# Kernel tuning notes

Measured on AMD Instinct MI355X. Metric: run time of the kernel, lower is better.

Reference implementation:

```python
import jax, jax.numpy as jnp
import numpy as np

B, T, F, H, OUT = 256, 256, 128, 1024, 128


def setup_inputs() -> dict:
    key = jax.random.key(0)
    ks = jax.random.split(key, 6)
    s_ih = 1.0 / np.sqrt(H)
    return {
        "x": jax.random.normal(ks[0], (B, T, F), dtype=jnp.float32),
        "h0": jnp.zeros((B, H), dtype=jnp.float32),
        "c0": jnp.zeros((B, H), dtype=jnp.float32),
        "W_ih": jax.random.normal(ks[1], (4 * H, F), dtype=jnp.float32) * s_ih,
        "W_hh": jax.random.normal(ks[2], (4 * H, H), dtype=jnp.float32) * s_ih,
        "b_ih": jax.random.normal(ks[3], (4 * H,), dtype=jnp.float32) * s_ih,
        "b_hh": jax.random.normal(ks[4], (4 * H,), dtype=jnp.float32) * s_ih,
        "W_fc": jax.random.normal(ks[5], (OUT, H), dtype=jnp.float32) * s_ih,
        "b_fc": jnp.zeros((OUT,), dtype=jnp.float32),
    }


def _lstm_scan(x, h0, c0, W_ih, W_hh, b_ih, b_hh):
    # Precompute input projections for all timesteps: [T, B, 4H]
    x_t = jnp.swapaxes(x, 0, 1)  # [T, B, F]
    x_proj = jnp.einsum('tbf,gf->tbg', x_t, W_ih) + b_ih + b_hh

    def step(carry, xp):
        h, c = carry
        gates = xp + h @ W_hh.T  # [B, 4H]
        i, f, g, o = jnp.split(gates, 4, axis=-1)  # PyTorch LSTMCell gate order
        i = jax.nn.sigmoid(i)
        f = jax.nn.sigmoid(f)
        g = jnp.tanh(g)
        o = jax.nn.sigmoid(o)
        c = f * c + i * g
        h = o * jnp.tanh(c)
        return (h, c), None

    (h, c), _ = jax.lax.scan(step, (h0, c0), x_proj)
    return h, c


def reference(x, h0, c0, W_ih, W_hh, b_ih, b_hh, W_fc, b_fc):
    h, c = _lstm_scan(x, h0, c0, W_ih, W_hh, b_ih, b_hh)
    sig_out = jax.nn.sigmoid(h)
    # Dropout is identity in eval/reference mode
    return sig_out @ W_fc.T + b_fc  # [B, OUT]
```

## Files before the change

kernel.cpp:

```cpp
#include <hip/hip_runtime.h>


typedef _Float16 f16x8 __attribute__((ext_vector_type(8)));
typedef float f32x16 __attribute__((ext_vector_type(16)));
typedef unsigned long long u64;

#define SCOPE_AGENT __HIP_MEMORY_SCOPE_AGENT

#define WS_WP    0ull
#define WS_BIAS  9437184ull
#define WS_XT    (WS_BIAS + 16384ull)
#define WS_HB    (WS_XT + 16777216ull)
#define WS_SIGH  (WS_HB + 4ull * 262144ull)
#define WS_BAR   (WS_SIGH + 1048576ull)

__device__ __forceinline__ unsigned short f2h(float f) {
  _Float16 h = (_Float16)f;
  return __builtin_bit_cast(unsigned short, h);
}

__device__ __forceinline__ float fast_sig(float x) {
  return __builtin_amdgcn_rcpf(1.f + __expf(-x));
}
__device__ __forceinline__ float fast_tanh(float x) {
  return __builtin_fmaf(2.f, fast_sig(2.f * x), -1.f);
}

__device__ __forceinline__ unsigned char h_enc(float v) {
  _Float16 gh = (_Float16)(v * 0.00390625f);
  unsigned m = __builtin_bit_cast(unsigned short, gh);
  unsigned r = m + 0x3fu + ((m >> 7) & 1u);
  return (unsigned char)(((m >> 8) & 0x80u) | ((r >> 7) & 0x7fu));
}

__device__ __forceinline__ f16x8 dq(u64 v) {
  unsigned w0 = (unsigned)v, w1 = (unsigned)(v >> 32);
  unsigned e0 = w0 & 0x00ff00ffu, o0 = (w0 >> 8) & 0x00ff00ffu;
  unsigned e1 = w1 & 0x00ff00ffu, o1 = (w1 >> 8) & 0x00ff00ffu;
  int4 t;
  t.x = (int)((e0 + (e0 & 0x00800080u)) << 7);
  t.y = (int)((o0 + (o0 & 0x00800080u)) << 7);
  t.z = (int)((e1 + (e1 & 0x00800080u)) << 7);
  t.w = (int)((o1 + (o1 & 0x00800080u)) << 7);
  return __builtin_bit_cast(f16x8, t);
}

__global__ void prep_pack(const float* __restrict__ W_ih, const float* __restrict__ W_hh,
                          const float* __restrict__ b_ih, const float* __restrict__ b_hh,
                          unsigned short* __restrict__ wp, float* __restrict__ bias) {
  unsigned i = blockIdx.x * 256u + threadIdx.x;
  if (i < 4718592u) {
    unsigned j = i & 7u;
    unsigned l = (i >> 3) & 63u;
    unsigned rest = i >> 9;
    unsigned q = rest % 18u;
    unsigned rest2 = rest / 18u;
    unsigned n = rest2 & 3u;
    unsigned rest3 = rest2 >> 2;
    unsigned w = rest3 & 3u;
    unsigned cg = rest3 >> 2;
    unsigned gcol = n * 1024u + cg * 32u + (l & 31u);
    unsigned khi = (l >> 5) * 8u;
    float v;
    if (q < 16u) {
      unsigned pj = (0x75643120u >> (4u * j)) & 0xfu;
      unsigned k = w * 256u + q * 16u + khi + pj;
      v = W_hh[(size_t)gcol * 1024u + k];
    } else {
      unsigned k = w * 32u + (q - 16u) * 16u + khi + j;
      v = W_ih[(size_t)gcol * 128u + k];
    }
    wp[i] = f2h(v * 256.0f);
  }
  if (i < 4096u) bias[i] = b_ih[i] + b_hh[i];
}

__global__ void prep_misc(const float* __restrict__ x, const float* __restrict__ h0,
                          unsigned short* __restrict__ xT, unsigned char* __restrict__ hb0,
                          unsigned* __restrict__ bar) {
  unsigned i = blockIdx.x * 256u + threadIdx.x;
  if (i < 8388608u) {
    unsigned f = i & 127u;
    unsigned b = (i >> 7) & 255u;
    unsigned t = i >> 15;
    xT[i] = f2h(x[((size_t)b * 256u + t) * 128u + f] * 0.00390625f);
  }
  if (i < 262144u) hb0[i] = h_enc(h0[i]);
  if (i < 768u) bar[i] = 0u;
}

__launch_bounds__(256, 1)
__global__ void lstm_main(const unsigned short* __restrict__ wp,
                          const float* __restrict__ bias,
                          const unsigned short* __restrict__ xT,
                          unsigned char* __restrict__ hb,
                          const float* __restrict__ c0,
                          float* __restrict__ sigh,
                          unsigned* __restrict__ bar) {
  extern __shared__ char lds[];
  char* stg = lds;
  float4* redv = (float4*)(lds + 32768);
  unsigned char* hst8 = (unsigned char*)(lds + 98304);

  const unsigned tid = threadIdx.x;
  const unsigned wg  = blockIdx.x;
  const unsigned w   = tid >> 6;
  const unsigned l   = tid & 63u;
  const unsigned rg  = wg >> 5;
  const unsigned cg  = wg & 31u;
  const unsigned lo5 = l & 31u;
  const unsigned hi  = l >> 5;

  int4 Braw[4][18];
  {
    const int4* wpv = (const int4*)wp;
    const unsigned wbase = (cg * 4u + w) * 4608u;
#pragma unroll
    for (int n = 0; n < 4; ++n) {
#pragma unroll
      for (int q = 0; q < 18; ++q) {
        Braw[n][q] = wpv[wbase + (unsigned)(n * 18 + q) * 64u + l];
      }
    }
  }

  float bias_v[4];
#pragma unroll
  for (int n = 0; n < 4; ++n) bias_v[n] = bias[(unsigned)n * 1024u + cg * 32u + lo5];

  const unsigned col = cg * 32u + lo5;
  float c_st[4];
  unsigned soff[4];
#pragma unroll
  for (int i = 0; i < 4; ++i) {
    unsigned r = rg * 32u + 8u * w + (unsigned)i + 4u * hi;
    soff[i] = r * 1024u + col;
    c_st[i] = c0[soff[i]];
  }

  const unsigned sgsrc0 = (rg * 32u + hi) * 1024u + w * 256u + lo5 * 8u;
  const unsigned sdst0  = w * 8192u + hi * 256u + lo5 * 8u;
  const unsigned frb = w * 8192u + lo5 * 256u + hi * 8u;
  const unsigned fxr = (lo5 & 7u) << 3;

  unsigned xb = ((rg * 32u + lo5) * 128u + w * 32u + hi * 8u) * 2u;

  const char* xbase = (const char*)xT;
  char* hbase = (char*)hb;
  unsigned* flags = &bar[rg * 32u];

  const unsigned srow = tid >> 3;
  const unsigned sseg = tid & 7u;
  const unsigned sgoff = (rg * 32u + srow) * 1024u + cg * 32u + sseg * 4u;

  int4 xr[2];
  xr[0] = *(const int4*)(xbase + xb);
  xr[1] = *(const int4*)(xbase + xb + 32u);

  for (unsigned t = 0; t < 256u; ++t) {
    const char* hrd = hbase + ((t & 3u) * 262144u);
    char* hwr = hbase + (((t + 1u) & 3u) * 262144u);

    u64 sa[16];
#pragma unroll
    for (int r = 0; r < 16; ++r)
      sa[r] = __hip_atomic_load((const u64*)(hrd + sgsrc0 + (unsigned)r * 2048u),
                                __ATOMIC_RELAXED, SCOPE_AGENT);

    f32x16 acc[4] = {};
#pragma unroll
    for (int qx = 0; qx < 2; ++qx) {
      f16x8 a = __builtin_bit_cast(f16x8, xr[qx]);
      acc[0] = __builtin_amdgcn_mfma_f32_32x32x16_f16(a, __builtin_bit_cast(f16x8, Braw[0][16 + qx]), acc[0], 0, 0, 0);
      acc[1] = __builtin_amdgcn_mfma_f32_32x32x16_f16(a, __builtin_bit_cast(f16x8, Braw[1][16 + qx]), acc[1], 0, 0, 0);
      acc[2] = __builtin_amdgcn_mfma_f32_32x32x16_f16(a, __builtin_bit_cast(f16x8, Braw[2][16 + qx]), acc[2], 0, 0, 0);
      acc[3] = __builtin_amdgcn_mfma_f32_32x32x16_f16(a, __builtin_bit_cast(f16x8, Braw[3][16 + qx]), acc[3], 0, 0, 0);
    }

#pragma unroll
    for (int r = 0; r < 16; ++r) {
      unsigned d = sdst0 + (unsigned)r * 512u;
      unsigned a = d ^ (((d >> 8) & 7u) << 3);
      *(u64*)(stg + a) = sa[r];
    }
    asm volatile("s_waitcnt lgkmcnt(0)" ::: "memory");

#pragma unroll
    for (int q = 0; q < 16; ++q) {
      unsigned a2 = (frb + (unsigned)q * 16u) ^ fxr;
      u64 hv = *(const u64*)(stg + a2);
      f16x8 a = dq(hv);
      acc[0] = __builtin_amdgcn_mfma_f32_32x32x16_f16(a, __builtin_bit_cast(f16x8, Braw[0][q]), acc[0], 0, 0, 0);
      acc[1] = __builtin_amdgcn_mfma_f32_32x32x16_f16(a, __builtin_bit_cast(f16x8, Braw[1][q]), acc[1], 0, 0, 0);
      acc[2] = __builtin_amdgcn_mfma_f32_32x32x16_f16(a, __builtin_bit_cast(f16x8, Braw[2][q]), acc[2], 0, 0, 0);
      acc[3] = __builtin_amdgcn_mfma_f32_32x32x16_f16(a, __builtin_bit_cast(f16x8, Braw[3][q]), acc[3], 0, 0, 0);
    }

#pragma unroll
    for (int n = 0; n < 4; ++n) {
#pragma unroll
      for (int c = 0; c < 4; ++c) {
        float4 v;
        v.x = acc[n][4 * c + 0]; v.y = acc[n][4 * c + 1];
        v.z = acc[n][4 * c + 2]; v.w = acc[n][4 * c + 3];
        redv[((w * 4u + (unsigned)n) * 4u + (unsigned)c) * 64u + l] = v;
      }
    }
    __syncthreads();

    float gv[4][4];
#pragma unroll
    for (int n = 0; n < 4; ++n) {
      float4 s; s.x = bias_v[n]; s.y = bias_v[n]; s.z = bias_v[n]; s.w = bias_v[n];
#pragma unroll
      for (int wo = 0; wo < 4; ++wo) {
        float4 v = redv[(((unsigned)wo * 4u + (unsigned)n) * 4u + w) * 64u + l];
        s.x += v.x; s.y += v.y; s.z += v.z; s.w += v.w;
      }
      gv[n][0] = s.x; gv[n][1] = s.y; gv[n][2] = s.z; gv[n][3] = s.w;
    }

    const bool last = (t == 255u);
#pragma unroll
    for (int i = 0; i < 4; ++i) {
      float ig = fast_sig(gv[0][i]);
      float fg = fast_sig(gv[1][i]);
      float gg = fast_tanh(gv[2][i]);
      float og = fast_sig(gv[3][i]);
      float cc = fg * c_st[i] + ig * gg;
      c_st[i] = cc;
      float hh = og * fast_tanh(cc);
      hst8[(8u * w + (unsigned)i + 4u * hi) * 32u + lo5] = h_enc(hh);
      if (last) sigh[soff[i]] = fast_sig(hh);
    }

    if (!last) {
      __syncthreads();
      {
        unsigned v = *(const unsigned*)(hst8 + srow * 32u + sseg * 4u);
        __hip_atomic_store((unsigned*)(hwr + sgoff), v, __ATOMIC_RELAXED, SCOPE_AGENT);
      }
      xb += 65536u;
      xr[0] = *(const int4*)(xbase + xb);
      xr[1] = *(const int4*)(xbase + xb + 32u);
      __syncthreads();
      if (tid == 0)
        __hip_atomic_store(&flags[cg], t + 1u, __ATOMIC_RELAXED, SCOPE_AGENT);
      {
        const unsigned tgt = t + 1u;
        const unsigned fidx = w * 8u + (l & 7u);
        for (;;) {
          unsigned f = __hip_atomic_load(&flags[fidx], __ATOMIC_RELAXED, SCOPE_AGENT);
          if (__all(f >= tgt)) break;
          __builtin_amdgcn_s_sleep(1);
        }
      }
    }
  }
}

__global__ void final_fc(const float* __restrict__ sigh, const float* __restrict__ W_fc,
                         const float* __restrict__ b_fc, float* __restrict__ out) {
  unsigned b = blockIdx.x;
  unsigned o = threadIdx.x;
  const float* hrow = sigh + (size_t)b * 1024u;
  const float* wrow = W_fc + (size_t)o * 1024u;
  float acc = b_fc[o];
#pragma unroll 8
  for (unsigned k = 0; k < 1024u; k += 4u) {
    float4 hv = *(const float4*)(hrow + k);
    float4 wv = *(const float4*)(wrow + k);
    acc += hv.x * wv.x + hv.y * wv.y + hv.z * wv.z + hv.w * wv.w;
  }
  out[b * 128u + o] = acc;
}

extern "C" void kernel_launch(void* const* d_in, const int* in_sizes, int n_in,
                              void* d_out, int out_size, void* d_ws, size_t ws_size,
                              hipStream_t stream) {
  (void)in_sizes; (void)n_in; (void)out_size; (void)ws_size;
  const float* x    = (const float*)d_in[0];
  const float* h0   = (const float*)d_in[1];
  const float* c0   = (const float*)d_in[2];
  const float* W_ih = (const float*)d_in[3];
  const float* W_hh = (const float*)d_in[4];
  const float* b_ih = (const float*)d_in[5];
  const float* b_hh = (const float*)d_in[6];
  const float* W_fc = (const float*)d_in[7];
  const float* b_fc = (const float*)d_in[8];

  char* ws = (char*)d_ws;
  unsigned short* wp   = (unsigned short*)(ws + WS_WP);
  float*          bias = (float*)(ws + WS_BIAS);
  unsigned short* xT   = (unsigned short*)(ws + WS_XT);
  unsigned char*  hb   = (unsigned char*)(ws + WS_HB);
  float*          sigh = (float*)(ws + WS_SIGH);
  unsigned*       bar  = (unsigned*)(ws + WS_BAR);
  float*          out  = (float*)d_out;

  prep_pack<<<18432, 256, 0, stream>>>(W_ih, W_hh, b_ih, b_hh, wp, bias);
  prep_misc<<<32768, 256, 0, stream>>>(x, h0, xT, hb, bar);
  lstm_main<<<256, 256, 99328, stream>>>(wp, bias, xT, hb, c0, sigh, bar);
  final_fc<<<256, 128, 0, stream>>>(sigh, W_fc, b_fc, out);
}
```

Baseline: 1.308 ms.

## Split batch into two interleaved halves with hash-verified speculative h reads

Each workgroup now processes two 16-row batch halves (A and B) in alternation, so the cross-workgroup exchange of one half overlaps with the compute of the other. The MFMA tiling changes from 32x32x16 to 16x16x32, and the weight packing is rearranged to match. The per-step flag barrier is replaced by speculative loads of the hidden-state tile, checked against a per-tile hash carrying the epoch. The code falls back to flag polling only when the hash does not match. The aim is to remove the global barrier latency from the recurrence's critical path. The cost is extra hashing arithmetic, and hash-based validation carries a small risk of a false match.

```diff
diff --git a/kernel.cpp b/kernel.cpp
--- a/kernel.cpp
+++ b/kernel.cpp
@@ -2,8 +2,9 @@
 
 
 typedef _Float16 f16x8 __attribute__((ext_vector_type(8)));
-typedef float f32x16 __attribute__((ext_vector_type(16)));
+typedef float f32x4 __attribute__((ext_vector_type(4)));
 typedef unsigned long long u64;
+typedef unsigned u32;
 
 #define SCOPE_AGENT __HIP_MEMORY_SCOPE_AGENT
 
@@ -11,28 +12,26 @@
 #define WS_BIAS  9437184ull
 #define WS_XT    (WS_BIAS + 16384ull)
 #define WS_HB    (WS_XT + 16777216ull)
-#define WS_SIGH  (WS_HB + 4ull * 262144ull)
+#define WS_HASH  (WS_HB + 1048576ull)
+#define WS_SIGH  (WS_HASH + 8192ull)
 #define WS_BAR   (WS_SIGH + 1048576ull)
 
 __device__ __forceinline__ unsigned short f2h(float f) {
   _Float16 h = (_Float16)f;
   return __builtin_bit_cast(unsigned short, h);
 }
-
 __device__ __forceinline__ float fast_sig(float x) {
   return __builtin_amdgcn_rcpf(1.f + __expf(-x));
 }
 __device__ __forceinline__ float fast_tanh(float x) {
   return __builtin_fmaf(2.f, fast_sig(2.f * x), -1.f);
 }
-
 __device__ __forceinline__ unsigned char h_enc(float v) {
   _Float16 gh = (_Float16)(v * 0.00390625f);
   unsigned m = __builtin_bit_cast(unsigned short, gh);
   unsigned r = m + 0x3fu + ((m >> 7) & 1u);
   return (unsigned char)(((m >> 8) & 0x80u) | ((r >> 7) & 0x7fu));
 }
-
 __device__ __forceinline__ f16x8 dq(u64 v) {
   unsigned w0 = (unsigned)v, w1 = (unsigned)(v >> 32);
   unsigned e0 = w0 & 0x00ff00ffu, o0 = (w0 >> 8) & 0x00ff00ffu;
@@ -45,6 +44,12 @@
   return __builtin_bit_cast(f16x8, t);
 }
 
+__device__ __forceinline__ u32 fold64(u64 v) {
+  return (u32)v ^ ((u32)(v >> 32) * 0x85EBCA77u);
+}
+#define HASH_INIT(EP, POS) (0x9E3779B9u * (u32)(EP) + (u32)(POS) * 0x7FEB352Du + 0x165667B1u)
+#define HASH_STEP(H, V, R)  ((((H) ^ fold64(V)) * 0x9E3779B1u) + (u32)(R))
+
 __global__ void prep_pack(const float* __restrict__ W_ih, const float* __restrict__ W_hh,
                           const float* __restrict__ b_ih, const float* __restrict__ b_hh,
                           unsigned short* __restrict__ wp, float* __restrict__ bias) {
@@ -53,22 +58,22 @@
     unsigned j = i & 7u;
     unsigned l = (i >> 3) & 63u;
     unsigned rest = i >> 9;
-    unsigned q = rest % 18u;
-    unsigned rest2 = rest / 18u;
-    unsigned n = rest2 & 3u;
-    unsigned rest3 = rest2 >> 2;
+    unsigned q = rest % 9u;
+    unsigned rest2 = rest / 9u;
+    unsigned ct = rest2 & 7u;
+    unsigned rest3 = rest2 >> 3;
     unsigned w = rest3 & 3u;
     unsigned cg = rest3 >> 2;
-    unsigned gcol = n * 1024u + cg * 32u + (l & 31u);
-    unsigned khi = (l >> 5) * 8u;
+    unsigned gcol = (ct >> 1) * 1024u + cg * 32u + (ct & 1u) * 16u + (l & 15u);
+    unsigned khi = (l >> 4) * 8u;
     float v;
-    if (q < 16u) {
+    if (q < 8u) {
       unsigned pj = (0x75643120u >> (4u * j)) & 0xfu;
-      unsigned k = w * 256u + q * 16u + khi + pj;
+      unsigned k = w * 256u + q * 32u + khi + pj;
       v = W_hh[(size_t)gcol * 1024u + k];
     } else {
-      unsigned k = w * 32u + (q - 16u) * 16u + khi + j;
-      v = W_ih[(size_t)gcol * 128u + k];
+      unsigned f = w * 32u + khi + j;
+      v = W_ih[(size_t)gcol * 128u + f];
     }
     wp[i] = f2h(v * 256.0f);
   }
@@ -76,7 +81,7 @@
 }
 
 __global__ void prep_misc(const float* __restrict__ x, const float* __restrict__ h0,
-                          unsigned short* __restrict__ xT, unsigned char* __restrict__ hb0,
+                          unsigned short* __restrict__ xT, unsigned char* __restrict__ hb,
                           unsigned* __restrict__ bar) {
   unsigned i = blockIdx.x * 256u + threadIdx.x;
   if (i < 8388608u) {
@@ -85,22 +90,76 @@
     unsigned t = i >> 15;
     xT[i] = f2h(x[((size_t)b * 256u + t) * 128u + f] * 0.00390625f);
   }
-  if (i < 262144u) hb0[i] = h_enc(h0[i]);
-  if (i < 768u) bar[i] = 0u;
-}
+  if (i < 262144u) {
+    unsigned col = i & 1023u;
+    unsigned grow = i >> 10;
+    unsigned g = grow >> 7;
+    unsigned rg = (grow >> 4) & 7u;
+    unsigned row = grow & 15u;
+    hb[((g * 4u + 0u) * 8u + rg) * 16384u + row * 1024u + col] = h_enc(h0[i]);
+  }
+  if (i < 512u) bar[i] = 0u;
+}
+
+__global__ void prep_hash(const unsigned char* __restrict__ hb, unsigned* __restrict__ hashes) {
+  unsigned id = blockIdx.x * 256u + threadIdx.x;
+  if (id >= 512u) return;
+  unsigned g = id >> 8, rg = (id >> 5) & 7u, cg = id & 31u;
+  const unsigned char* base = hb + ((g * 4u + 0u) * 8u + rg) * 16384u;
+  u32 tile = 0u;
+  for (unsigned pos = 0; pos < 8u; ++pos) {
+    u32 h = HASH_INIT(0u, pos);
+    for (unsigned r = 0; r < 8u; ++r) {
+      u64 v = *(const u64*)(base + ((pos >> 2) + 2u * r) * 1024u + cg * 32u + (pos & 3u) * 8u);
+      h = HASH_STEP(h, v, r);
+    }
+    tile ^= h;
+  }
+  hashes[((g * 4u + 0u) * 8u + rg) * 32u + cg] = tile;
+}
+
+#define SPEC_LOAD(SA, HA, G, SLOT) do {                                          \
+    const char* _b = (const char*)hbase + (((G)*4u + (SLOT))*8u + rg)*16384u     \
+                     + hi*1024u + w*256u + lo5*8u;                               \
+    for (int _r = 0; _r < 8; ++_r)                                               \
+      SA[_r] = __hip_atomic_load((const u64*)(_b + (unsigned)_r*2048u),          \
+                                 __ATOMIC_RELAXED, SCOPE_AGENT);                 \
+    HA = __hip_atomic_load(hashes + (((G)*4u + (SLOT))*8u + rg)*32u              \
+                           + w*8u + (lo5 >> 2), __ATOMIC_RELAXED, SCOPE_AGENT);  \
+  } while (0)
+
+#define VERIFY(SA, HA, EPOCH, OK) do {                                           \
+    u32 _h = HASH_INIT((EPOCH), pos);                                            \
+    for (int _r = 0; _r < 8; ++_r) _h = HASH_STEP(_h, SA[_r], _r);               \
+    _h ^= (u32)__shfl_xor((int)_h, 1, 64);                                       \
+    _h ^= (u32)__shfl_xor((int)_h, 2, 64);                                       \
+    _h ^= (u32)__shfl_xor((int)_h, 32, 64);                                      \
+    OK = __all(_h == (HA));                                                      \
+  } while (0)
+
+#define POLL(FL, TGT) do {                                                       \
+    for (;;) {                                                                   \
+      unsigned _f = __hip_atomic_load((FL) + w*8u + (l & 7u),                    \
+                                      __ATOMIC_RELAXED, SCOPE_AGENT);            \
+      if (__all(_f >= (TGT))) break;                                             \
+      __builtin_amdgcn_s_sleep(1);                                               \
+    }                                                                            \
+  } while (0)
 
 __launch_bounds__(256, 1)
 __global__ void lstm_main(const unsigned short* __restrict__ wp,
                           const float* __restrict__ bias,
                           const unsigned short* __restrict__ xT,
                           unsigned char* __restrict__ hb,
+                          unsigned* __restrict__ hashes,
                           const float* __restrict__ c0,
                           float* __restrict__ sigh,
                           unsigned* __restrict__ bar) {
   extern __shared__ char lds[];
-  char* stg = lds;
-  float4* redv = (float4*)(lds + 32768);
-  unsigned char* hst8 = (unsigned char*)(lds + 98304);
+  float4* redv = (float4*)(lds + 16384);
+  float*  redf = (float*)(lds + 16384);
+  unsigned char* hstA = (unsigned char*)(lds + 49152);
+  unsigned char* hstB = (unsigned char*)(lds + 49664);
 
   const unsigned tid = threadIdx.x;
   const unsigned wg  = blockIdx.x;
@@ -110,150 +169,228 @@
   const unsigned cg  = wg & 31u;
   const unsigned lo5 = l & 31u;
   const unsigned hi  = l >> 5;
-
-  int4 Braw[4][18];
+  const unsigned l15 = l & 15u;
+  const unsigned l4  = l >> 4;
+  const unsigned pos = (hi << 2) | (lo5 & 3u);
+  const unsigned row = l4 * 4u + w;
+
+  int4 Braw[8][9];
   {
     const int4* wpv = (const int4*)wp;
     const unsigned wbase = (cg * 4u + w) * 4608u;
 #pragma unroll
-    for (int n = 0; n < 4; ++n) {
-#pragma unroll
-      for (int q = 0; q < 18; ++q) {
-        Braw[n][q] = wpv[wbase + (unsigned)(n * 18 + q) * 64u + l];
-      }
-    }
-  }
-
-  float bias_v[4];
-#pragma unroll
-  for (int n = 0; n < 4; ++n) bias_v[n] = bias[(unsigned)n * 1024u + cg * 32u + lo5];
-
-  const unsigned col = cg * 32u + lo5;
-  float c_st[4];
-  unsigned soff[4];
-#pragma unroll
-  for (int i = 0; i < 4; ++i) {
-    unsigned r = rg * 32u + 8u * w + (unsigned)i + 4u * hi;
-    soff[i] = r * 1024u + col;
-    c_st[i] = c0[soff[i]];
-  }
-
-  const unsigned sgsrc0 = (rg * 32u + hi) * 1024u + w * 256u + lo5 * 8u;
-  const unsigned sdst0  = w * 8192u + hi * 256u + lo5 * 8u;
-  const unsigned frb = w * 8192u + lo5 * 256u + hi * 8u;
-  const unsigned fxr = (lo5 & 7u) << 3;
-
-  unsigned xb = ((rg * 32u + lo5) * 128u + w * 32u + hi * 8u) * 2u;
+    for (int ct = 0; ct < 8; ++ct)
+#pragma unroll
+      for (int q = 0; q < 9; ++q)
+        Braw[ct][q] = wpv[wbase + (unsigned)(ct * 9 + q) * 64u + l];
+  }
+
+  float bias_v[8];
+#pragma unroll
+  for (int ct = 0; ct < 8; ++ct)
+    bias_v[ct] = bias[(unsigned)(ct >> 1) * 1024u + cg * 32u + (unsigned)(ct & 1) * 16u + l15];
+
+  const unsigned gbA = rg * 16u, gbB = 128u + rg * 16u;
+  float cA[2], cB[2];
+  unsigned soffA[2], soffB[2];
+#pragma unroll
+  for (int hh = 0; hh < 2; ++hh) {
+    soffA[hh] = (gbA + row) * 1024u + cg * 32u + (unsigned)hh * 16u + l15;
+    soffB[hh] = (gbB + row) * 1024u + cg * 32u + (unsigned)hh * 16u + l15;
+    cA[hh] = c0[soffA[hh]];
+    cB[hh] = c0[soffB[hh]];
+  }
 
   const char* xbase = (const char*)xT;
-  char* hbase = (char*)hb;
-  unsigned* flags = &bar[rg * 32u];
-
-  const unsigned srow = tid >> 3;
-  const unsigned sseg = tid & 7u;
-  const unsigned sgoff = (rg * 32u + srow) * 1024u + cg * 32u + sseg * 4u;
-
-  int4 xr[2];
-  xr[0] = *(const int4*)(xbase + xb);
-  xr[1] = *(const int4*)(xbase + xb + 32u);
+  const unsigned xoffA = ((gbA + l15) * 128u + w * 32u + l4 * 8u) * 2u;
+  const unsigned xoffB = ((gbB + l15) * 128u + w * 32u + l4 * 8u) * 2u;
+  unsigned char* hbase = hb;
+  unsigned* flagsA = &bar[rg * 32u];
+  unsigned* flagsB = &bar[256u + rg * 32u];
+
+  const unsigned fb = w * 4096u + l15 * 256u + l4 * 8u;
+  const unsigned fx = (l15 & 7u) << 3;
+
+  u64 saA[8], saB[8];
+  u32 haA, haB;
+  int4 xrA, xrB;
+
+  SPEC_LOAD(saA, haA, 0u, 0u);
+  xrA = *(const int4*)(xbase + xoffA);
+  xrB = *(const int4*)(xbase + xoffB);
 
   for (unsigned t = 0; t < 256u; ++t) {
-    const char* hrd = hbase + ((t & 3u) * 262144u);
-    char* hwr = hbase + (((t + 1u) & 3u) * 262144u);
-
-    u64 sa[16];
-#pragma unroll
-    for (int r = 0; r < 16; ++r)
-      sa[r] = __hip_atomic_load((const u64*)(hrd + sgsrc0 + (unsigned)r * 2048u),
-                                __ATOMIC_RELAXED, SCOPE_AGENT);
-
-    f32x16 acc[4] = {};
-#pragma unroll
-    for (int qx = 0; qx < 2; ++qx) {
-      f16x8 a = __builtin_bit_cast(f16x8, xr[qx]);
-      acc[0] = __builtin_amdgcn_mfma_f32_32x32x16_f16(a, __builtin_bit_cast(f16x8, Braw[0][16 + qx]), acc[0], 0, 0, 0);
-      acc[1] = __builtin_amdgcn_mfma_f32_32x32x16_f16(a, __builtin_bit_cast(f16x8, Braw[1][16 + qx]), acc[1], 0, 0, 0);
-      acc[2] = __builtin_amdgcn_mfma_f32_32x32x16_f16(a, __builtin_bit_cast(f16x8, Braw[2][16 + qx]), acc[2], 0, 0, 0);
-      acc[3] = __builtin_amdgcn_mfma_f32_32x32x16_f16(a, __builtin_bit_cast(f16x8, Braw[3][16 + qx]), acc[3], 0, 0, 0);
-    }
-
-#pragma unroll
-    for (int r = 0; r < 16; ++r) {
-      unsigned d = sdst0 + (unsigned)r * 512u;
-      unsigned a = d ^ (((d >> 8) & 7u) << 3);
-      *(u64*)(stg + a) = sa[r];
-    }
-    asm volatile("s_waitcnt lgkmcnt(0)" ::: "memory");
-
-#pragma unroll
-    for (int q = 0; q < 16; ++q) {
-      unsigned a2 = (frb + (unsigned)q * 16u) ^ fxr;
-      u64 hv = *(const u64*)(stg + a2);
+    const bool last = (t == 255u);
+    const unsigned slot = t & 3u, wslot = (t + 1u) & 3u;
+
+    {
+      bool ok; VERIFY(saA, haA, t, ok);
+      if (!ok) {
+        SPEC_LOAD(saA, haA, 0u, slot);
+        VERIFY(saA, haA, t, ok);
+        if (!ok) { POLL(flagsA, t); SPEC_LOAD(saA, haA, 0u, slot); }
+      }
+    }
+    SPEC_LOAD(saB, haB, 1u, slot);
+
+#pragma unroll
+    for (int r = 0; r < 8; ++r) {
+      unsigned d = w * 4096u + (hi + 2u * (unsigned)r) * 256u + lo5 * 8u;
+      *(u64*)(lds + (d ^ (((d >> 8) & 7u) << 3))) = saA[r];
+    }
+    f32x4 acc[8] = {};
+    {
+      f16x8 a = __builtin_bit_cast(f16x8, xrA);
+#pragma unroll
+      for (int ct = 0; ct < 8; ++ct)
+        acc[ct] = __builtin_amdgcn_mfma_f32_16x16x32_f16(a, __builtin_bit_cast(f16x8, Braw[ct][8]), acc[ct], 0, 0, 0);
+    }
+#pragma unroll
+    for (int q = 0; q < 8; ++q) {
+      u64 hv = *(const u64*)(lds + ((fb + (unsigned)q * 32u) ^ fx));
       f16x8 a = dq(hv);
-      acc[0] = __builtin_amdgcn_mfma_f32_32x32x16_f16(a, __builtin_bit_cast(f16x8, Braw[0][q]), acc[0], 0, 0, 0);
-      acc[1] = __builtin_amdgcn_mfma_f32_32x32x16_f16(a, __builtin_bit_cast(f16x8, Braw[1][q]), acc[1], 0, 0, 0);
-      acc[2] = __builtin_amdgcn_mfma_f32_32x32x16_f16(a, __builtin_bit_cast(f16x8, Braw[2][q]), acc[2], 0, 0, 0);
-      acc[3] = __builtin_amdgcn_mfma_f32_32x32x16_f16(a, __builtin_bit_cast(f16x8, Braw[3][q]), acc[3], 0, 0, 0);
-    }
-
-#pragma unroll
-    for (int n = 0; n < 4; ++n) {
-#pragma unroll
-      for (int c = 0; c < 4; ++c) {
-        float4 v;
-        v.x = acc[n][4 * c + 0]; v.y = acc[n][4 * c + 1];
-        v.z = acc[n][4 * c + 2]; v.w = acc[n][4 * c + 3];
-        redv[((w * 4u + (unsigned)n) * 4u + (unsigned)c) * 64u + l] = v;
-      }
+#pragma unroll
+      for (int ct = 0; ct < 8; ++ct)
+        acc[ct] = __builtin_amdgcn_mfma_f32_16x16x32_f16(a, __builtin_bit_cast(f16x8, Braw[ct][q]), acc[ct], 0, 0, 0);
+    }
+#pragma unroll
+    for (int ct = 0; ct < 8; ++ct) {
+      float4 v; v.x = acc[ct][0]; v.y = acc[ct][1]; v.z = acc[ct][2]; v.w = acc[ct][3];
+      redv[(w * 8u + (unsigned)ct) * 64u + l] = v;
     }
     __syncthreads();
-
-    float gv[4][4];
-#pragma unroll
-    for (int n = 0; n < 4; ++n) {
-      float4 s; s.x = bias_v[n]; s.y = bias_v[n]; s.z = bias_v[n]; s.w = bias_v[n];
-#pragma unroll
-      for (int wo = 0; wo < 4; ++wo) {
-        float4 v = redv[(((unsigned)wo * 4u + (unsigned)n) * 4u + w) * 64u + l];
-        s.x += v.x; s.y += v.y; s.z += v.z; s.w += v.w;
-      }
-      gv[n][0] = s.x; gv[n][1] = s.y; gv[n][2] = s.z; gv[n][3] = s.w;
-    }
-
-    const bool last = (t == 255u);
-#pragma unroll
-    for (int i = 0; i < 4; ++i) {
-      float ig = fast_sig(gv[0][i]);
-      float fg = fast_sig(gv[1][i]);
-      float gg = fast_tanh(gv[2][i]);
-      float og = fast_sig(gv[3][i]);
-      float cc = fg * c_st[i] + ig * gg;
-      c_st[i] = cc;
-      float hh = og * fast_tanh(cc);
-      hst8[(8u * w + (unsigned)i + 4u * hi) * 32u + lo5] = h_enc(hh);
-      if (last) sigh[soff[i]] = fast_sig(hh);
-    }
-
+    float gv[8];
+#pragma unroll
+    for (int ct = 0; ct < 8; ++ct) {
+      float s = bias_v[ct];
+#pragma unroll
+      for (int wo = 0; wo < 4; ++wo)
+        s += redf[(((unsigned)wo * 8u + (unsigned)ct) * 64u + l) * 4u + w];
+      gv[ct] = s;
+    }
+#pragma unroll
+    for (int hh = 0; hh < 2; ++hh) {
+      float ig = fast_sig(gv[0 * 2 + hh]);
+      float fg = fast_sig(gv[1 * 2 + hh]);
+      float gg = fast_tanh(gv[2 * 2 + hh]);
+      float og = fast_sig(gv[3 * 2 + hh]);
+      float cc = fg * cA[hh] + ig * gg;
+      cA[hh] = cc;
+      float hhv = og * fast_tanh(cc);
+      hstA[row * 32u + (unsigned)hh * 16u + l15] = h_enc(hhv);
+      if (last) sigh[soffA[hh]] = fast_sig(hhv);
+    }
+    __syncthreads();
     if (!last) {
+      if (tid < 128u) {
+        unsigned v = *(const unsigned*)(hstA + (tid >> 3) * 32u + (tid & 7u) * 4u);
+        char* dst = (char*)hbase + ((0u * 4u + wslot) * 8u + rg) * 16384u
+                    + (tid >> 3) * 1024u + cg * 32u + (tid & 7u) * 4u;
+        __hip_atomic_store((unsigned*)dst, v, __ATOMIC_RELAXED, SCOPE_AGENT);
+      }
+      if (tid < 8u) {
+        u32 h = HASH_INIT(t + 1u, tid);
+#pragma unroll
+        for (int r = 0; r < 8; ++r) {
+          u64 v = *(const u64*)(hstA + ((tid >> 2) + 2u * (unsigned)r) * 32u + (tid & 3u) * 8u);
+          h = HASH_STEP(h, v, r);
+        }
+        h ^= (u32)__shfl_xor((int)h, 1, 64);
+        h ^= (u32)__shfl_xor((int)h, 2, 64);
+        h ^= (u32)__shfl_xor((int)h, 4, 64);
+        if (tid == 0u)
+          __hip_atomic_store(hashes + ((0u * 4u + wslot) * 8u + rg) * 32u + cg, h,
+                             __ATOMIC_RELAXED, SCOPE_AGENT);
+      }
+    }
+
+    {
+      bool ok; VERIFY(saB, haB, t, ok);
+      if (!ok) {
+        SPEC_LOAD(saB, haB, 1u, slot);
+        VERIFY(saB, haB, t, ok);
+        if (!ok) { POLL(flagsB, t); SPEC_LOAD(saB, haB, 1u, slot); }
+      }
+    }
+    if (!last) {
+      SPEC_LOAD(saA, haA, 0u, wslot);
+      xrA = *(const int4*)(xbase + xoffA + (t + 1u) * 65536u);
+    }
+
+#pragma unroll
+    for (int r = 0; r < 8; ++r) {
+      unsigned d = w * 4096u + (hi + 2u * (unsigned)r) * 256u + lo5 * 8u;
+      *(u64*)(lds + (d ^ (((d >> 8) & 7u) << 3))) = saB[r];
+    }
+    f32x4 accB[8] = {};
+    {
+      f16x8 a = __builtin_bit_cast(f16x8, xrB);
+#pragma unroll
+      for (int ct = 0; ct < 8; ++ct)
+        accB[ct] = __builtin_amdgcn_mfma_f32_16x16x32_f16(a, __builtin_bit_cast(f16x8, Braw[ct][8]), accB[ct], 0, 0, 0);
+    }
+#pragma unroll
+    for (int q = 0; q < 8; ++q) {
+      u64 hv = *(const u64*)(lds + ((fb + (unsigned)q * 32u) ^ fx));
+      f16x8 a = dq(hv);
+#pragma unroll
+      for (int ct = 0; ct < 8; ++ct)
+        accB[ct] = __builtin_amdgcn_mfma_f32_16x16x32_f16(a, __builtin_bit_cast(f16x8, Braw[ct][q]), accB[ct], 0, 0, 0);
+    }
+    __syncthreads();
+#pragma unroll
+    for (int ct = 0; ct < 8; ++ct) {
+      float4 v; v.x = accB[ct][0]; v.y = accB[ct][1]; v.z = accB[ct][2]; v.w = accB[ct][3];
+      redv[(w * 8u + (unsigned)ct) * 64u + l] = v;
+    }
+    __syncthreads();
+#pragma unroll
+    for (int ct = 0; ct < 8; ++ct) {
+      float s = bias_v[ct];
+#pragma unroll
+      for (int wo = 0; wo < 4; ++wo)
+        s += redf[(((unsigned)wo * 8u + (unsigned)ct) * 64u + l) * 4u + w];
+      gv[ct] = s;
+    }
+#pragma unroll
+    for (int hh = 0; hh < 2; ++hh) {
+      float ig = fast_sig(gv[0 * 2 + hh]);
+      float fg = fast_sig(gv[1 * 2 + hh]);
+      float gg = fast_tanh(gv[2 * 2 + hh]);
+      float og = fast_sig(gv[3 * 2 + hh]);
+      float cc = fg * cB[hh] + ig * gg;
+      cB[hh] = cc;
+      float hhv = og * fast_tanh(cc);
+      hstB[row * 32u + (unsigned)hh * 16u + l15] = h_enc(hhv);
+      if (last) sigh[soffB[hh]] = fast_sig(hhv);
+    }
+    __syncthreads();
+    if (!last) {
+      if (tid < 128u) {
+        unsigned v = *(const unsigned*)(hstB + (tid >> 3) * 32u + (tid & 7u) * 4u);
+        char* dst = (char*)hbase + ((1u * 4u + wslot) * 8u + rg) * 16384u
+                    + (tid >> 3) * 1024u + cg * 32u + (tid & 7u) * 4u;
+        __hip_atomic_store((unsigned*)dst, v, __ATOMIC_RELAXED, SCOPE_AGENT);
+      }
+      if (tid < 8u) {
+        u32 h = HASH_INIT(t + 1u, tid);
+#pragma unroll
+        for (int r = 0; r < 8; ++r) {
+          u64 v = *(const u64*)(hstB + ((tid >> 2) + 2u * (unsigned)r) * 32u + (tid & 3u) * 8u);
+          h = HASH_STEP(h, v, r);
+        }
+        h ^= (u32)__shfl_xor((int)h, 1, 64);
+        h ^= (u32)__shfl_xor((int)h, 2, 64);
+        h ^= (u32)__shfl_xor((int)h, 4, 64);
+        if (tid == 0u)
+          __hip_atomic_store(hashes + ((1u * 4u + wslot) * 8u + rg) * 32u + cg, h,
+                             __ATOMIC_RELAXED, SCOPE_AGENT);
+      }
+      xrB = *(const int4*)(xbase + xoffB + (t + 1u) * 65536u);
       __syncthreads();
-      {
-        unsigned v = *(const unsigned*)(hst8 + srow * 32u + sseg * 4u);
-        __hip_atomic_store((unsigned*)(hwr + sgoff), v, __ATOMIC_RELAXED, SCOPE_AGENT);
-      }
-      xb += 65536u;
-      xr[0] = *(const int4*)(xbase + xb);
-      xr[1] = *(const int4*)(xbase + xb + 32u);
-      __syncthreads();
-      if (tid == 0)
-        __hip_atomic_store(&flags[cg], t + 1u, __ATOMIC_RELAXED, SCOPE_AGENT);
-      {
-        const unsigned tgt = t + 1u;
-        const unsigned fidx = w * 8u + (l & 7u);
-        for (;;) {
-          unsigned f = __hip_atomic_load(&flags[fidx], __ATOMIC_RELAXED, SCOPE_AGENT);
-          if (__all(f >= tgt)) break;
-          __builtin_amdgcn_s_sleep(1);
-        }
+      if (tid == 0u) {
+        __hip_atomic_store(&flagsA[cg], t + 1u, __ATOMIC_RELAXED, SCOPE_AGENT);
+        __hip_atomic_store(&flagsB[cg], t + 1u, __ATOMIC_RELAXED, SCOPE_AGENT);
       }
     }
   }
@@ -294,12 +431,14 @@
   float*          bias = (float*)(ws + WS_BIAS);
   unsigned short* xT   = (unsigned short*)(ws + WS_XT);
   unsigned char*  hb   = (unsigned char*)(ws + WS_HB);
+  unsigned*       hashes = (unsigned*)(ws + WS_HASH);
   float*          sigh = (float*)(ws + WS_SIGH);
   unsigned*       bar  = (unsigned*)(ws + WS_BAR);
   float*          out  = (float*)d_out;
 
   prep_pack<<<18432, 256, 0, stream>>>(W_ih, W_hh, b_ih, b_hh, wp, bias);
   prep_misc<<<32768, 256, 0, stream>>>(x, h0, xT, hb, bar);
-  lstm_main<<<256, 256, 99328, stream>>>(wp, bias, xT, hb, c0, sigh, bar);
+  prep_hash<<<2, 256, 0, stream>>>(hb, hashes);
+  lstm_main<<<256, 256, 50176, stream>>>(wp, bias, xT, hb, hashes, c0, sigh, bar);
   final_fc<<<256, 128, 0, stream>>>(sigh, W_fc, b_fc, out);
 }
```

New measurement: 1.715 ms. 1.31x slower.

## Retile LSTM workgroups to 64 rows by 16 hidden columns per block

Applied to the files above, without the earlier changes.

Changes the persistent LSTM decomposition from 8 row groups by 32 column groups to 4 row groups by 64 column groups. Each workgroup now handles 64 batch rows and 16 hidden units (all four gates), halving register-resident weights per wave while doubling A-tile reuse across two M tiles. The h exchange buffer is reorganized per row group, and gate results go through an extra LDS transpose so each thread packs 4 outputs into one 32-bit store. This trades more LDS traffic, a larger LDS allocation and 64-way flag polling for fewer workgroups synchronizing per row group and better MFMA reuse.

```diff
diff --git a/kernel.cpp b/kernel.cpp
--- a/kernel.cpp
+++ b/kernel.cpp
@@ -4,6 +4,7 @@
 typedef _Float16 f16x8 __attribute__((ext_vector_type(8)));
 typedef float f32x16 __attribute__((ext_vector_type(16)));
 typedef unsigned long long u64;
+typedef unsigned u32;
 
 #define SCOPE_AGENT __HIP_MEMORY_SCOPE_AGENT
 
@@ -11,28 +12,25 @@
 #define WS_BIAS  9437184ull
 #define WS_XT    (WS_BIAS + 16384ull)
 #define WS_HB    (WS_XT + 16777216ull)
-#define WS_SIGH  (WS_HB + 4ull * 262144ull)
+#define WS_SIGH  (WS_HB + 1048576ull)
 #define WS_BAR   (WS_SIGH + 1048576ull)
 
 __device__ __forceinline__ unsigned short f2h(float f) {
   _Float16 h = (_Float16)f;
   return __builtin_bit_cast(unsigned short, h);
 }
-
 __device__ __forceinline__ float fast_sig(float x) {
   return __builtin_amdgcn_rcpf(1.f + __expf(-x));
 }
 __device__ __forceinline__ float fast_tanh(float x) {
   return __builtin_fmaf(2.f, fast_sig(2.f * x), -1.f);
 }
-
 __device__ __forceinline__ unsigned char h_enc(float v) {
   _Float16 gh = (_Float16)(v * 0.00390625f);
   unsigned m = __builtin_bit_cast(unsigned short, gh);
   unsigned r = m + 0x3fu + ((m >> 7) & 1u);
   return (unsigned char)(((m >> 8) & 0x80u) | ((r >> 7) & 0x7fu));
 }
-
 __device__ __forceinline__ f16x8 dq(u64 v) {
   unsigned w0 = (unsigned)v, w1 = (unsigned)(v >> 32);
   unsigned e0 = w0 & 0x00ff00ffu, o0 = (w0 >> 8) & 0x00ff00ffu;
@@ -44,6 +42,11 @@
   t.w = (int)((o1 + (o1 & 0x00800080u)) << 7);
   return __builtin_bit_cast(f16x8, t);
 }
+__device__ __forceinline__ void lds_barrier() {
+  asm volatile("s_waitcnt lgkmcnt(0)" ::: "memory");
+  __builtin_amdgcn_s_barrier();
+  asm volatile("" ::: "memory");
+}
 
 __global__ void prep_pack(const float* __restrict__ W_ih, const float* __restrict__ W_hh,
                           const float* __restrict__ b_ih, const float* __restrict__ b_hh,
@@ -55,11 +58,12 @@
     unsigned rest = i >> 9;
     unsigned q = rest % 18u;
     unsigned rest2 = rest / 18u;
-    unsigned n = rest2 & 3u;
-    unsigned rest3 = rest2 >> 2;
+    unsigned nt = rest2 & 1u;
+    unsigned rest3 = rest2 >> 1;
     unsigned w = rest3 & 3u;
     unsigned cg = rest3 >> 2;
-    unsigned gcol = n * 1024u + cg * 32u + (l & 31u);
+    unsigned u = nt * 32u + (l & 31u);
+    unsigned gcol = (u >> 4) * 1024u + cg * 16u + (u & 15u);
     unsigned khi = (l >> 5) * 8u;
     float v;
     if (q < 16u) {
@@ -67,8 +71,8 @@
       unsigned k = w * 256u + q * 16u + khi + pj;
       v = W_hh[(size_t)gcol * 1024u + k];
     } else {
-      unsigned k = w * 32u + (q - 16u) * 16u + khi + j;
-      v = W_ih[(size_t)gcol * 128u + k];
+      unsigned f = w * 32u + (q - 16u) * 16u + khi + j;
+      v = W_ih[(size_t)gcol * 128u + f];
     }
     wp[i] = f2h(v * 256.0f);
   }
@@ -76,7 +80,7 @@
 }
 
 __global__ void prep_misc(const float* __restrict__ x, const float* __restrict__ h0,
-                          unsigned short* __restrict__ xT, unsigned char* __restrict__ hb0,
+                          unsigned short* __restrict__ xT, unsigned char* __restrict__ hb,
                           unsigned* __restrict__ bar) {
   unsigned i = blockIdx.x * 256u + threadIdx.x;
   if (i < 8388608u) {
@@ -85,8 +89,14 @@
     unsigned t = i >> 15;
     xT[i] = f2h(x[((size_t)b * 256u + t) * 128u + f] * 0.00390625f);
   }
-  if (i < 262144u) hb0[i] = h_enc(h0[i]);
-  if (i < 768u) bar[i] = 0u;
+  if (i < 262144u) {
+    unsigned col = i & 1023u;
+    unsigned grow = i >> 10;
+    unsigned rg = grow >> 6;
+    unsigned row = grow & 63u;
+    hb[rg * 65536u + row * 1024u + col] = h_enc(h0[i]);
+  }
+  if (i < 512u) bar[i] = 0u;
 }
 
 __launch_bounds__(256, 1)
@@ -98,160 +108,177 @@
                           float* __restrict__ sigh,
                           unsigned* __restrict__ bar) {
   extern __shared__ char lds[];
-  char* stg = lds;
-  float4* redv = (float4*)(lds + 32768);
-  unsigned char* hst8 = (unsigned char*)(lds + 98304);
+  float4* redv = (float4*)(lds + 65536);
+  float4* Sf4  = (float4*)(lds + 131072);
+  float*  Sff  = (float*)(lds + 131072);
 
   const unsigned tid = threadIdx.x;
   const unsigned wg  = blockIdx.x;
   const unsigned w   = tid >> 6;
   const unsigned l   = tid & 63u;
-  const unsigned rg  = wg >> 5;
-  const unsigned cg  = wg & 31u;
+  const unsigned rg  = wg >> 6;
+  const unsigned cg  = wg & 63u;
   const unsigned lo5 = l & 31u;
   const unsigned hi  = l >> 5;
 
-  int4 Braw[4][18];
+  int4 Braw[2][18];
   {
     const int4* wpv = (const int4*)wp;
-    const unsigned wbase = (cg * 4u + w) * 4608u;
-#pragma unroll
-    for (int n = 0; n < 4; ++n) {
-#pragma unroll
-      for (int q = 0; q < 18; ++q) {
-        Braw[n][q] = wpv[wbase + (unsigned)(n * 18 + q) * 64u + l];
-      }
-    }
-  }
-
-  float bias_v[4];
-#pragma unroll
-  for (int n = 0; n < 4; ++n) bias_v[n] = bias[(unsigned)n * 1024u + cg * 32u + lo5];
-
-  const unsigned col = cg * 32u + lo5;
+    const unsigned wbase = (cg * 4u + w) * 2304u;
+#pragma unroll
+    for (int nt = 0; nt < 2; ++nt)
+#pragma unroll
+      for (int q = 0; q < 18; ++q)
+        Braw[nt][q] = wpv[wbase + (unsigned)(nt * 18 + q) * 64u + l];
+  }
+
+  const unsigned crow = tid >> 2;
+  const unsigned hcB  = (tid & 3u) * 4u;
+  float4 bias_v[4];
+#pragma unroll
+  for (int n = 0; n < 4; ++n)
+    bias_v[n] = *(const float4*)(bias + (unsigned)n * 1024u + cg * 16u + hcB);
+  const unsigned gsoff = (rg * 64u + crow) * 1024u + cg * 16u + hcB;
   float c_st[4];
-  unsigned soff[4];
-#pragma unroll
-  for (int i = 0; i < 4; ++i) {
-    unsigned r = rg * 32u + 8u * w + (unsigned)i + 4u * hi;
-    soff[i] = r * 1024u + col;
-    c_st[i] = c0[soff[i]];
-  }
-
-  const unsigned sgsrc0 = (rg * 32u + hi) * 1024u + w * 256u + lo5 * 8u;
-  const unsigned sdst0  = w * 8192u + hi * 256u + lo5 * 8u;
-  const unsigned frb = w * 8192u + lo5 * 256u + hi * 8u;
-  const unsigned fxr = (lo5 & 7u) << 3;
-
-  unsigned xb = ((rg * 32u + lo5) * 128u + w * 32u + hi * 8u) * 2u;
+  {
+    float4 c4 = *(const float4*)(c0 + gsoff);
+    c_st[0] = c4.x; c_st[1] = c4.y; c_st[2] = c4.z; c_st[3] = c4.w;
+  }
+  const unsigned mt_c = crow >> 5;
+  const unsigned r_c  = crow & 31u;
+  const unsigned hi2  = (r_c >> 2) & 1u;
+  const unsigned e_c  = (r_c & 3u) + 4u * (r_c >> 3);
+
+  const unsigned sgsrc0 = hi * 1024u + w * 256u + lo5 * 8u;
+  const unsigned frow0 = w * 16384u + lo5 * 256u;
+  const unsigned frow1 = w * 16384u + (32u + lo5) * 256u;
+  const unsigned fxr   = (lo5 & 15u) << 3;
+
+  unsigned xoff[2][2];
+#pragma unroll
+  for (int mt = 0; mt < 2; ++mt)
+#pragma unroll
+    for (int qx = 0; qx < 2; ++qx)
+      xoff[mt][qx] = ((rg * 64u + (unsigned)mt * 32u + lo5) * 128u
+                      + w * 32u + (unsigned)qx * 16u + hi * 8u) * 2u;
 
   const char* xbase = (const char*)xT;
   char* hbase = (char*)hb;
-  unsigned* flags = &bar[rg * 32u];
-
-  const unsigned srow = tid >> 3;
-  const unsigned sseg = tid & 7u;
-  const unsigned sgoff = (rg * 32u + srow) * 1024u + cg * 32u + sseg * 4u;
-
-  int4 xr[2];
-  xr[0] = *(const int4*)(xbase + xb);
-  xr[1] = *(const int4*)(xbase + xb + 32u);
+  unsigned* flags = &bar[rg * 64u];
+
+  u64 sa[32];
+  int4 xr[2][2];
+#pragma unroll
+  for (int mt = 0; mt < 2; ++mt)
+#pragma unroll
+    for (int qx = 0; qx < 2; ++qx)
+      xr[mt][qx] = *(const int4*)(xbase + xoff[mt][qx]);
 
   for (unsigned t = 0; t < 256u; ++t) {
-    const char* hrd = hbase + ((t & 3u) * 262144u);
-    char* hwr = hbase + (((t + 1u) & 3u) * 262144u);
-
-    u64 sa[16];
-#pragma unroll
-    for (int r = 0; r < 16; ++r)
+    const bool last = (t == 255u);
+    const unsigned slot = t & 3u, wslot = (t + 1u) & 3u;
+    const char* hrd = hbase + slot * 262144u + rg * 65536u;
+    char* hwr = hbase + wslot * 262144u + rg * 65536u;
+
+#pragma unroll
+    for (int r = 0; r < 32; ++r)
       sa[r] = __hip_atomic_load((const u64*)(hrd + sgsrc0 + (unsigned)r * 2048u),
                                 __ATOMIC_RELAXED, SCOPE_AGENT);
 
-    f32x16 acc[4] = {};
+    f32x16 acc00 = {}, acc01 = {}, acc10 = {}, acc11 = {};
 #pragma unroll
     for (int qx = 0; qx < 2; ++qx) {
-      f16x8 a = __builtin_bit_cast(f16x8, xr[qx]);
-      acc[0] = __builtin_amdgcn_mfma_f32_32x32x16_f16(a, __builtin_bit_cast(f16x8, Braw[0][16 + qx]), acc[0], 0, 0, 0);
-      acc[1] = __builtin_amdgcn_mfma_f32_32x32x16_f16(a, __builtin_bit_cast(f16x8, Braw[1][16 + qx]), acc[1], 0, 0, 0);
-      acc[2] = __builtin_amdgcn_mfma_f32_32x32x16_f16(a, __builtin_bit_cast(f16x8, Braw[2][16 + qx]), acc[2], 0, 0, 0);
-      acc[3] = __builtin_amdgcn_mfma_f32_32x32x16_f16(a, __builtin_bit_cast(f16x8, Braw[3][16 + qx]), acc[3], 0, 0, 0);
-    }
-
-#pragma unroll
-    for (int r = 0; r < 16; ++r) {
-      unsigned d = sdst0 + (unsigned)r * 512u;
-      unsigned a = d ^ (((d >> 8) & 7u) << 3);
-      *(u64*)(stg + a) = sa[r];
+      f16x8 a0 = __builtin_bit_cast(f16x8, xr[0][qx]);
+      f16x8 a1 = __builtin_bit_cast(f16x8, xr[1][qx]);
+      acc00 = __builtin_amdgcn_mfma_f32_32x32x16_f16(a0, __builtin_bit_cast(f16x8, Braw[0][16 + qx]), acc00, 0, 0, 0);
+      acc01 = __builtin_amdgcn_mfma_f32_32x32x16_f16(a0, __builtin_bit_cast(f16x8, Braw[1][16 + qx]), acc01, 0, 0, 0);
+      acc10 = __builtin_amdgcn_mfma_f32_32x32x16_f16(a1, __builtin_bit_cast(f16x8, Braw[0][16 + qx]), acc10, 0, 0, 0);
+      acc11 = __builtin_amdgcn_mfma_f32_32x32x16_f16(a1, __builtin_bit_cast(f16x8, Braw[1][16 + qx]), acc11, 0, 0, 0);
+    }
+
+#pragma unroll
+    for (int r = 0; r < 32; ++r) {
+      unsigned rr = hi + 2u * (unsigned)r;
+      unsigned d = w * 16384u + rr * 256u + ((lo5 * 8u) ^ ((rr & 15u) << 3));
+      *(u64*)(lds + d) = sa[r];
     }
     asm volatile("s_waitcnt lgkmcnt(0)" ::: "memory");
 
 #pragma unroll
     for (int q = 0; q < 16; ++q) {
-      unsigned a2 = (frb + (unsigned)q * 16u) ^ fxr;
-      u64 hv = *(const u64*)(stg + a2);
-      f16x8 a = dq(hv);
-      acc[0] = __builtin_amdgcn_mfma_f32_32x32x16_f16(a, __builtin_bit_cast(f16x8, Braw[0][q]), acc[0], 0, 0, 0);
-      acc[1] = __builtin_amdgcn_mfma_f32_32x32x16_f16(a, __builtin_bit_cast(f16x8, Braw[1][q]), acc[1], 0, 0, 0);
-      acc[2] = __builtin_amdgcn_mfma_f32_32x32x16_f16(a, __builtin_bit_cast(f16x8, Braw[2][q]), acc[2], 0, 0, 0);
-      acc[3] = __builtin_amdgcn_mfma_f32_32x32x16_f16(a, __builtin_bit_cast(f16x8, Braw[3][q]), acc[3], 0, 0, 0);
-    }
-
-#pragma unroll
-    for (int n = 0; n < 4; ++n) {
-#pragma unroll
-      for (int c = 0; c < 4; ++c) {
-        float4 v;
-        v.x = acc[n][4 * c + 0]; v.y = acc[n][4 * c + 1];
-        v.z = acc[n][4 * c + 2]; v.w = acc[n][4 * c + 3];
-        redv[((w * 4u + (unsigned)n) * 4u + (unsigned)c) * 64u + l] = v;
-      }
+      unsigned kb = ((unsigned)q * 16u + hi * 8u);
+      f16x8 a0 = dq(*(const u64*)(lds + frow0 + (kb ^ fxr)));
+      f16x8 a1 = dq(*(const u64*)(lds + frow1 + (kb ^ fxr)));
+      acc00 = __builtin_amdgcn_mfma_f32_32x32x16_f16(a0, __builtin_bit_cast(f16x8, Braw[0][q]), acc00, 0, 0, 0);
+      acc01 = __builtin_amdgcn_mfma_f32_32x32x16_f16(a0, __builtin_bit_cast(f16x8, Braw[1][q]), acc01, 0, 0, 0);
+      acc10 = __builtin_amdgcn_mfma_f32_32x32x16_f16(a1, __builtin_bit_cast(f16x8, Braw[0][q]), acc10, 0, 0, 0);
+      acc11 = __builtin_amdgcn_mfma_f32_32x32x16_f16(a1, __builtin_bit_cast(f16x8, Braw[1][q]), acc11, 0, 0, 0);
+    }
+
+#pragma unroll
+    for (int c = 0; c < 4; ++c) {
+      float4 v0; v0.x = acc00[4*c]; v0.y = acc00[4*c+1]; v0.z = acc00[4*c+2]; v0.w = acc00[4*c+3];
+      float4 v1; v1.x = acc01[4*c]; v1.y = acc01[4*c+1]; v1.z = acc01[4*c+2]; v1.w = acc01[4*c+3];
+      float4 v2; v2.x = acc10[4*c]; v2.y = acc10[4*c+1]; v2.z = acc10[4*c+2]; v2.w = acc10[4*c+3];
+      float4 v3; v3.x = acc11[4*c]; v3.y = acc11[4*c+1]; v3.z = acc11[4*c+2]; v3.w = acc11[4*c+3];
+      redv[((w * 4u + 0u) * 4u + (unsigned)c) * 64u + l] = v0;
+      redv[((w * 4u + 1u) * 4u + (unsigned)c) * 64u + l] = v1;
+      redv[((w * 4u + 2u) * 4u + (unsigned)c) * 64u + l] = v2;
+      redv[((w * 4u + 3u) * 4u + (unsigned)c) * 64u + l] = v3;
     }
     __syncthreads();
 
-    float gv[4][4];
-#pragma unroll
-    for (int n = 0; n < 4; ++n) {
-      float4 s; s.x = bias_v[n]; s.y = bias_v[n]; s.z = bias_v[n]; s.w = bias_v[n];
-#pragma unroll
-      for (int wo = 0; wo < 4; ++wo) {
-        float4 v = redv[(((unsigned)wo * 4u + (unsigned)n) * 4u + w) * 64u + l];
+#pragma unroll
+    for (int c = 0; c < 4; ++c) {
+      float4 s = redv[((0u * 4u + w) * 4u + (unsigned)c) * 64u + l];
+#pragma unroll
+      for (int wo = 1; wo < 4; ++wo) {
+        float4 v = redv[(((unsigned)wo * 4u + w) * 4u + (unsigned)c) * 64u + l];
         s.x += v.x; s.y += v.y; s.z += v.z; s.w += v.w;
       }
-      gv[n][0] = s.x; gv[n][1] = s.y; gv[n][2] = s.z; gv[n][3] = s.w;
-    }
-
-    const bool last = (t == 255u);
-#pragma unroll
-    for (int i = 0; i < 4; ++i) {
-      float ig = fast_sig(gv[0][i]);
-      float fg = fast_sig(gv[1][i]);
-      float gg = fast_tanh(gv[2][i]);
-      float og = fast_sig(gv[3][i]);
-      float cc = fg * c_st[i] + ig * gg;
-      c_st[i] = cc;
-      float hh = og * fast_tanh(cc);
-      hst8[(8u * w + (unsigned)i + 4u * hi) * 32u + lo5] = h_enc(hh);
-      if (last) sigh[soff[i]] = fast_sig(hh);
+      Sf4[(w * 4u + (unsigned)c) * 64u + l] = s;
+    }
+    lds_barrier();
+
+    u32 pk = 0u;
+#pragma unroll
+    for (int p = 0; p < 4; ++p) {
+      float gv[4];
+#pragma unroll
+      for (int n = 0; n < 4; ++n) {
+        unsigned u = (unsigned)n * 16u + hcB + (unsigned)p;
+        unsigned tile = mt_c * 2u + (u >> 5);
+        unsigned l2 = (u & 31u) + 32u * hi2;
+        gv[n] = Sff[((tile * 4u + (e_c >> 2)) * 64u + l2) * 4u + (e_c & 3u)];
+      }
+      float ig = fast_sig(gv[0] + ((const float*)&bias_v[0])[p]);
+      float fg = fast_sig(gv[1] + ((const float*)&bias_v[1])[p]);
+      float gg = fast_tanh(gv[2] + ((const float*)&bias_v[2])[p]);
+      float og = fast_sig(gv[3] + ((const float*)&bias_v[3])[p]);
+      float cc = fg * c_st[p] + ig * gg;
+      c_st[p] = cc;
+      float hhv = og * fast_tanh(cc);
+      pk |= (u32)h_enc(hhv) << (8 * p);
+      if (last) sigh[gsoff + (unsigned)p] = fast_sig(hhv);
     }
 
     if (!last) {
-      __syncthreads();
-      {
-        unsigned v = *(const unsigned*)(hst8 + srow * 32u + sseg * 4u);
-        __hip_atomic_store((unsigned*)(hwr + sgoff), v, __ATOMIC_RELAXED, SCOPE_AGENT);
-      }
-      xb += 65536u;
-      xr[0] = *(const int4*)(xbase + xb);
-      xr[1] = *(const int4*)(xbase + xb + 32u);
+      __hip_atomic_store((u32*)(hwr + crow * 1024u + cg * 16u + hcB), pk,
+                         __ATOMIC_RELAXED, SCOPE_AGENT);
+#pragma unroll
+      for (int mt = 0; mt < 2; ++mt)
+#pragma unroll
+        for (int qx = 0; qx < 2; ++qx)
+          xr[mt][qx] = *(const int4*)(xbase + xoff[mt][qx] + (t + 1u) * 65536u);
       __syncthreads();
       if (tid == 0)
         __hip_atomic_store(&flags[cg], t + 1u, __ATOMIC_RELAXED, SCOPE_AGENT);
       {
         const unsigned tgt = t + 1u;
-        const unsigned fidx = w * 8u + (l & 7u);
+        const unsigned fidx = w * 16u + (l & 15u);
         for (;;) {
           unsigned f = __hip_atomic_load(&flags[fidx], __ATOMIC_RELAXED, SCOPE_AGENT);
-          if (__all(f >= tgt)) break;
+          if (__all(l >= 16u || f >= tgt)) break;
           __builtin_amdgcn_s_sleep(1);
         }
       }
@@ -300,6 +327,6 @@
 
   prep_pack<<<18432, 256, 0, stream>>>(W_ih, W_hh, b_ih, b_hh, wp, bias);
   prep_misc<<<32768, 256, 0, stream>>>(x, h0, xT, hb, bar);
-  lstm_main<<<256, 256, 99328, stream>>>(wp, bias, xT, hb, c0, sigh, bar);
+  lstm_main<<<256, 256, 147456, stream>>>(wp, bias, xT, hb, c0, sigh, bar);
   final_fc<<<256, 128, 0, stream>>>(sigh, W_fc, b_fc, out);
 }
```

Result: slower. 2.061 ms (+57.6%).
